# Kernel optimization log

Hardware: AMD Instinct MI355X
Metric: run time of the kernel (lower is better)

The kernel has to match this reference:

```python
import jax, jax.numpy as jnp
import numpy as np

B, T, F, H = 2048, 256, 64, 128


def setup_inputs() -> dict:
    key = jax.random.key(0)
    ks = jax.random.split(key, 9)
    s = 0.1  # small init scale for stable recurrence
    return {
        "x": jax.random.normal(ks[0], (B, T, F), dtype=jnp.float32),
        "W_ih": jax.random.normal(ks[1], (4 * H, F), dtype=jnp.float32) * s,
        "W_hh": jax.random.normal(ks[2], (4 * H, H), dtype=jnp.float32) * s,
        "b_ih": jax.random.normal(ks[3], (4 * H,), dtype=jnp.float32) * s,
        "b_hh": jax.random.normal(ks[4], (4 * H,), dtype=jnp.float32) * s,
        "W1": jax.random.normal(ks[5], (32, H), dtype=jnp.float32) * s,
        "b1": jax.random.normal(ks[6], (32,), dtype=jnp.float32) * s,
        "W2": jax.random.normal(ks[7], (1, 32), dtype=jnp.float32) * s,
        "b2": jax.random.normal(ks[8], (1,), dtype=jnp.float32) * s,
    }


def reference(x, W_ih, W_hh, b_ih, b_hh, W1, b1, W2, b2):
    # Single-layer LSTM (PyTorch gate order i, f, g, o), take last hidden state.
    Bsz, Tlen, _ = x.shape
    Hdim = W_hh.shape[1]
    xt = jnp.swapaxes(x, 0, 1)  # [T, B, F]
    bias = b_ih + b_hh  # [4H]

    def step(carry, xb):
        h, c = carry
        gates = xb @ W_ih.T + h @ W_hh.T + bias  # [B, 4H]
        i, f, g, o = jnp.split(gates, 4, axis=-1)
        i = jax.nn.sigmoid(i)
        f = jax.nn.sigmoid(f)
        g = jnp.tanh(g)
        o = jax.nn.sigmoid(o)
        c = f * c + i * g
        h = o * jnp.tanh(c)
        return (h, c), None

    h0 = jnp.zeros((Bsz, Hdim), dtype=x.dtype)
    c0 = jnp.zeros((Bsz, Hdim), dtype=x.dtype)
    (h_last, _), _ = jax.lax.scan(step, (h0, c0), xt)

    # head: Linear(H,32) -> ReLU -> Linear(32,1) -> Sigmoid -> squeeze(-1)
    z = jax.nn.relu(h_last @ W1.T + b1)
    return jax.nn.sigmoid(z @ W2.T + b2)[:, 0]
```

## Files before the change

### kernel.cpp

```cpp
#include <hip/hip_runtime.h>


#define Bsz   2048
#define Tlen  256
#define Fdim  64
#define Hdim  128
#define ROWS  8
#define NTH   512
#define TILE_E 512
#define NKT   6
#define BUF_E (NKT * TILE_E)

using bf16x8 = __attribute__((ext_vector_type(8))) __bf16;
using f32x4  = __attribute__((ext_vector_type(4))) float;

__device__ __forceinline__ float fast_rcp(float x) {
#if __has_builtin(__builtin_amdgcn_rcpf)
    return __builtin_amdgcn_rcpf(x);
#else
    return 1.0f / x;
#endif
}
__device__ __forceinline__ float fast_exp2(float x) {
#if __has_builtin(__builtin_amdgcn_exp2f)
    return __builtin_amdgcn_exp2f(x);
#else
    return exp2f(x);
#endif
}
#define LOG2E  1.4426950408889634f
#define LOG2E2 2.8853900817779268f

__device__ __forceinline__ bf16x8 cvt8(float4 a, float4 b) {
    bf16x8 r;
    r[0]=(__bf16)a.x; r[1]=(__bf16)a.y; r[2]=(__bf16)a.z; r[3]=(__bf16)a.w;
    r[4]=(__bf16)b.x; r[5]=(__bf16)b.y; r[6]=(__bf16)b.z; r[7]=(__bf16)b.w;
    return r;
}

__device__ __forceinline__ int frag_elem(int row, int k) {
    return (k >> 5) * TILE_E + ((((k >> 3) & 3) * 16 + row) * 8) + (k & 7);
}

__global__ __launch_bounds__(NTH, 2)
void lstm_fused(const float* __restrict__ x,
                const float* __restrict__ W_ih,
                const float* __restrict__ W_hh,
                const float* __restrict__ b_ih,
                const float* __restrict__ b_hh,
                const float* __restrict__ W1,
                const float* __restrict__ b1,
                const float* __restrict__ W2,
                const float* __restrict__ b2,
                float* __restrict__ out)
{
    __shared__ __bf16 Abuf[2][BUF_E];
    __shared__ float  hlast[ROWS * Hdim];
    __shared__ float  zbuf[ROWS * 32];

    const int tid  = threadIdx.x;
    const int w    = tid >> 6;
    const int lane = tid & 63;
    const int quad = lane >> 4;
    const int l16  = lane & 15;
    const int b0   = blockIdx.x * ROWS;
    const bool hiq = (quad >= 2);

    bf16x8 bwx[2][4], bwh[4][4];
    #pragma unroll
    for (int kt = 0; kt < NKT; ++kt) {
        const int k0 = kt * 32 + quad * 8;
        #pragma unroll
        for (int g = 0; g < 4; ++g) {
            const int n = g * Hdim + w * 16 + l16;
            const float* p = (kt < 2) ? (W_ih + (size_t)n * Fdim + k0)
                                      : (W_hh + (size_t)n * Hdim + (k0 - Fdim));
            float4 lo = *(const float4*)p;
            float4 hi = *(const float4*)(p + 4);
            bf16x8 r = cvt8(lo, hi);
            if (kt < 2) bwx[kt][g] = r; else bwh[kt - 2][g] = r;
        }
    }
    f32x4 biasf[4];
    #pragma unroll
    for (int g = 0; g < 4; ++g) {
        const int n = g * Hdim + w * 16 + l16;
        const float bv = b_ih[n] + b_hh[n];
        biasf[g] = (f32x4){bv, bv, bv, bv};
    }

    const bool sx_on  = tid < 256;
    const int  sx_row = tid & 7;
    const int  sx_fp  = (tid >> 3) & 31;
    const int  f0     = 2 * sx_fp;
    const float* xrp  = x + (size_t)(b0 + sx_row) * (Tlen * Fdim) + f0;
    const int sx_e0 = frag_elem(sx_row,     f0);
    const int sx_e1 = frag_elem(sx_row + 8, f0);

    const int r0  = (quad >> 1) * 2;
    const int brb = (quad & 1) * 4 + r0;
    const int hc  = 16 * w + l16;
    const int h_e0a = frag_elem(brb,         Fdim + hc);
    const int h_e0b = frag_elem(brb + 8,     Fdim + hc);
    const int h_e1a = frag_elem(brb + 1,     Fdim + hc);
    const int h_e1b = frag_elem(brb + 1 + 8, Fdim + hc);

    #pragma unroll
    for (int i = 0; i < BUF_E / NTH; ++i)
        Abuf[0][tid + i * NTH] = (__bf16)0.0f;
    __syncthreads();
    float2 xpA = make_float2(0.f, 0.f);
    float2 xpB = make_float2(0.f, 0.f);
    if (sx_on) {
        float2 v1 = *(const float2*)(xrp + Fdim);
        __bf16 a1[2] = {(__bf16)v1.x, (__bf16)v1.y};
        *(uint*)&Abuf[0][sx_e0] = *(uint*)a1;
        *(uint*)&Abuf[0][sx_e1] = *(uint*)a1;
        xpA = *(const float2*)(xrp + 2 * Fdim);
        xpB = *(const float2*)(xrp + 3 * Fdim);
    }
    f32x4 xacc[4];
    {
        const float* x0p = x + (size_t)(b0 + (l16 & 7)) * (Tlen * Fdim) + quad * 8;
        float4 a0 = *(const float4*)(x0p);
        float4 a1 = *(const float4*)(x0p + 4);
        float4 a2 = *(const float4*)(x0p + 32);
        float4 a3 = *(const float4*)(x0p + 36);
        bf16x8 xi0 = cvt8(a0, a1), xi1 = cvt8(a2, a3);
        #pragma unroll
        for (int g = 0; g < 4; ++g) {
            f32x4 tmp = __builtin_amdgcn_mfma_f32_16x16x32_bf16(xi0, bwx[0][g], biasf[g], 0, 0, 0);
            xacc[g]   = __builtin_amdgcn_mfma_f32_16x16x32_bf16(xi1, bwx[1][g], tmp, 0, 0, 0);
        }
    }
    __syncthreads();

    float cc0 = 0.0f, cc1 = 0.0f;

    auto step = [&](int t, const __bf16* __restrict__ rb,
                    __bf16* __restrict__ wbf, float2& xstage) {
        bf16x8 hf[4];
        #pragma unroll
        for (int kt = 0; kt < 4; ++kt)
            hf[kt] = *(const bf16x8*)&rb[(2 + kt) * TILE_E + lane * 8];
        bf16x8 xf0 = *(const bf16x8*)&rb[lane * 8];
        bf16x8 xf1 = *(const bf16x8*)&rb[TILE_E + lane * 8];

        float2 xcur = xstage;
        if (sx_on && (t + 4) < Tlen)
            xstage = *(const float2*)(xrp + (size_t)(t + 4) * Fdim);

        f32x4 acc[4];
        #pragma unroll
        for (int g = 0; g < 4; ++g)
            acc[g] = __builtin_amdgcn_mfma_f32_16x16x32_bf16(hf[0], bwh[0][g], xacc[g], 0, 0, 0);
        #pragma unroll
        for (int kt = 1; kt < 4; ++kt) {
            #pragma unroll
            for (int g = 0; g < 4; ++g)
                acc[g] = __builtin_amdgcn_mfma_f32_16x16x32_bf16(hf[kt], bwh[kt][g], acc[g], 0, 0, 0);
        }

        if ((t + 1) < Tlen) {
            #pragma unroll
            for (int g = 0; g < 4; ++g) {
                f32x4 tmp = __builtin_amdgcn_mfma_f32_16x16x32_bf16(xf0, bwx[0][g], biasf[g], 0, 0, 0);
                xacc[g]   = __builtin_amdgcn_mfma_f32_16x16x32_bf16(xf1, bwx[1][g], tmp, 0, 0, 0);
            }
        }

        if (sx_on && (t + 2) < Tlen) {
            __bf16 xa[2] = {(__bf16)xcur.x, (__bf16)xcur.y};
            *(uint*)&wbf[sx_e0] = *(uint*)xa;
            *(uint*)&wbf[sx_e1] = *(uint*)xa;
        }

        __builtin_amdgcn_sched_barrier(0);

        {
            float gi = hiq ? acc[0][2] : acc[0][0];
            float gf = hiq ? acc[1][2] : acc[1][0];
            float gg = hiq ? acc[2][2] : acc[2][0];
            float go = hiq ? acc[3][2] : acc[3][0];
            float ei = fast_exp2(-LOG2E  * gi);
            float ef = fast_exp2(-LOG2E  * gf);
            float eg = fast_exp2(-LOG2E2 * gg);
            float eo = fast_exp2(-LOG2E  * go);
            float a = 1.0f + ef, b = 1.0f + ei, d = 1.0f + eg;
            float bd  = b * d;
            float num = cc0 * bd + a * (1.0f - eg);
            cc0 = num * fast_rcp(a * bd);
            float ec = fast_exp2(-LOG2E2 * cc0);
            float h  = (1.0f - ec) * fast_rcp((1.0f + eo) * (1.0f + ec));
            __bf16 hb = (__bf16)h;
            wbf[h_e0a] = hb;
            wbf[h_e0b] = hb;
            if (t == Tlen - 1) hlast[brb * Hdim + hc] = h;
        }
        {
            float gi = hiq ? acc[0][3] : acc[0][1];
            float gf = hiq ? acc[1][3] : acc[1][1];
            float gg = hiq ? acc[2][3] : acc[2][1];
            float go = hiq ? acc[3][3] : acc[3][1];
            float ei = fast_exp2(-LOG2E  * gi);
            float ef = fast_exp2(-LOG2E  * gf);
            float eg = fast_exp2(-LOG2E2 * gg);
            float eo = fast_exp2(-LOG2E  * go);
            float a = 1.0f + ef, b = 1.0f + ei, d = 1.0f + eg;
            float bd  = b * d;
            float num = cc1 * bd + a * (1.0f - eg);
            cc1 = num * fast_rcp(a * bd);
            float ec = fast_exp2(-LOG2E2 * cc1);
            float h  = (1.0f - ec) * fast_rcp((1.0f + eo) * (1.0f + ec));
            __bf16 hb = (__bf16)h;
            wbf[h_e1a] = hb;
            wbf[h_e1b] = hb;
            if (t == Tlen - 1) hlast[(brb + 1) * Hdim + hc] = h;
        }

        asm volatile("s_waitcnt lgkmcnt(0)" ::: "memory");
        __builtin_amdgcn_s_barrier();
        __builtin_amdgcn_sched_barrier(0);
    };

    for (int t = 0; t < Tlen; t += 2) {
        step(t,     Abuf[0], Abuf[1], xpA);
        step(t + 1, Abuf[1], Abuf[0], xpB);
    }

    if (tid < ROWS * 32) {
        const int b = tid >> 5, n = tid & 31;
        const float4* w4 = (const float4*)(W1 + n * Hdim);
        const float4* h4 = (const float4*)(hlast + b * Hdim);
        float s = b1[n];
        #pragma unroll
        for (int kk = 0; kk < Hdim / 4; ++kk) {
            float4 wv = w4[kk];
            float4 hv = h4[kk];
            s += wv.x * hv.x + wv.y * hv.y + wv.z * hv.z + wv.w * hv.w;
        }
        zbuf[b * 32 + n] = fmaxf(s, 0.0f);
    }
    __syncthreads();
    if (tid < ROWS) {
        float s = b2[0];
        #pragma unroll
        for (int n = 0; n < 32; ++n) s += zbuf[tid * 32 + n] * W2[n];
        float e = fast_exp2(-LOG2E * s);
        out[b0 + tid] = fast_rcp(1.0f + e);
    }
}

extern "C" void kernel_launch(void* const* d_in, const int* in_sizes, int n_in,
                              void* d_out, int out_size, void* d_ws, size_t ws_size,
                              hipStream_t stream) {
    const float* x    = (const float*)d_in[0];
    const float* W_ih = (const float*)d_in[1];
    const float* W_hh = (const float*)d_in[2];
    const float* b_ih = (const float*)d_in[3];
    const float* b_hh = (const float*)d_in[4];
    const float* W1   = (const float*)d_in[5];
    const float* b1   = (const float*)d_in[6];
    const float* W2   = (const float*)d_in[7];
    const float* b2   = (const float*)d_in[8];
    float* out = (float*)d_out;

    dim3 grid(Bsz / ROWS), block(NTH);
    lstm_fused<<<grid, block, 0, stream>>>(x, W_ih, W_hh, b_ih, b_hh, W1, b1, W2, b2, out);
}
```

Baseline: 342.9 us.

## Load x fragments directly from global into registers instead of staging through LDS

```diff
diff --git a/kernel.cpp b/kernel.cpp
--- a/kernel.cpp
+++ b/kernel.cpp
@@ -8,8 +8,8 @@
 #define ROWS  8
 #define NTH   512
 #define TILE_E 512
-#define NKT   6
-#define BUF_E (NKT * TILE_E)
+#define NKT_H 4
+#define BUF_E (NKT_H * TILE_E)
 
 using bf16x8 = __attribute__((ext_vector_type(8))) __bf16;
 using f32x4  = __attribute__((ext_vector_type(4))) float;
@@ -68,7 +68,7 @@
 
     bf16x8 bwx[2][4], bwh[4][4];
     #pragma unroll
-    for (int kt = 0; kt < NKT; ++kt) {
+    for (int kt = 0; kt < 6; ++kt) {
         const int k0 = kt * 32 + quad * 8;
         #pragma unroll
         for (int g = 0; g < 4; ++g) {
@@ -89,43 +89,35 @@
         biasf[g] = (f32x4){bv, bv, bv, bv};
     }
 
-    const bool sx_on  = tid < 256;
-    const int  sx_row = tid & 7;
-    const int  sx_fp  = (tid >> 3) & 31;
-    const int  f0     = 2 * sx_fp;
-    const float* xrp  = x + (size_t)(b0 + sx_row) * (Tlen * Fdim) + f0;
-    const int sx_e0 = frag_elem(sx_row,     f0);
-    const int sx_e1 = frag_elem(sx_row + 8, f0);
+    const float* xq = x + (size_t)(b0 + (l16 & 7)) * (Tlen * Fdim) + quad * 8;
 
     const int r0  = (quad >> 1) * 2;
     const int brb = (quad & 1) * 4 + r0;
     const int hc  = 16 * w + l16;
-    const int h_e0a = frag_elem(brb,         Fdim + hc);
-    const int h_e0b = frag_elem(brb + 8,     Fdim + hc);
-    const int h_e1a = frag_elem(brb + 1,     Fdim + hc);
-    const int h_e1b = frag_elem(brb + 1 + 8, Fdim + hc);
+    const int h_e0a = frag_elem(brb,         hc);
+    const int h_e0b = frag_elem(brb + 8,     hc);
+    const int h_e1a = frag_elem(brb + 1,     hc);
+    const int h_e1b = frag_elem(brb + 1 + 8, hc);
 
     #pragma unroll
     for (int i = 0; i < BUF_E / NTH; ++i)
         Abuf[0][tid + i * NTH] = (__bf16)0.0f;
-    __syncthreads();
-    float2 xpA = make_float2(0.f, 0.f);
-    float2 xpB = make_float2(0.f, 0.f);
-    if (sx_on) {
-        float2 v1 = *(const float2*)(xrp + Fdim);
-        __bf16 a1[2] = {(__bf16)v1.x, (__bf16)v1.y};
-        *(uint*)&Abuf[0][sx_e0] = *(uint*)a1;
-        *(uint*)&Abuf[0][sx_e1] = *(uint*)a1;
-        xpA = *(const float2*)(xrp + 2 * Fdim);
-        xpB = *(const float2*)(xrp + 3 * Fdim);
+
+    float4 xA0, xA1, xA2, xA3, xB0, xB1, xB2, xB3;
+    xB0 = xB1 = xB2 = xB3 = make_float4(0.f, 0.f, 0.f, 0.f);
+    {
+        const float* p = xq + (size_t)1 * Fdim;
+        xA0 = *(const float4*)(p);
+        xA1 = *(const float4*)(p + 4);
+        xA2 = *(const float4*)(p + 32);
+        xA3 = *(const float4*)(p + 36);
     }
     f32x4 xacc[4];
     {
-        const float* x0p = x + (size_t)(b0 + (l16 & 7)) * (Tlen * Fdim) + quad * 8;
-        float4 a0 = *(const float4*)(x0p);
-        float4 a1 = *(const float4*)(x0p + 4);
-        float4 a2 = *(const float4*)(x0p + 32);
-        float4 a3 = *(const float4*)(x0p + 36);
+        float4 a0 = *(const float4*)(xq);
+        float4 a1 = *(const float4*)(xq + 4);
+        float4 a2 = *(const float4*)(xq + 32);
+        float4 a3 = *(const float4*)(xq + 36);
         bf16x8 xi0 = cvt8(a0, a1), xi1 = cvt8(a2, a3);
         #pragma unroll
         for (int g = 0; g < 4; ++g) {
@@ -138,41 +130,40 @@
     float cc0 = 0.0f, cc1 = 0.0f;
 
     auto step = [&](int t, const __bf16* __restrict__ rb,
-                    __bf16* __restrict__ wbf, float2& xstage) {
+                    __bf16* __restrict__ wbf,
+                    float4& xh0, float4& xh1, float4& xh2, float4& xh3,
+                    float4& xl0, float4& xl1, float4& xl2, float4& xl3) {
         bf16x8 hf[4];
         #pragma unroll
-        for (int kt = 0; kt < 4; ++kt)
-            hf[kt] = *(const bf16x8*)&rb[(2 + kt) * TILE_E + lane * 8];
-        bf16x8 xf0 = *(const bf16x8*)&rb[lane * 8];
-        bf16x8 xf1 = *(const bf16x8*)&rb[TILE_E + lane * 8];
-
-        float2 xcur = xstage;
-        if (sx_on && (t + 4) < Tlen)
-            xstage = *(const float2*)(xrp + (size_t)(t + 4) * Fdim);
+        for (int kt = 0; kt < NKT_H; ++kt)
+            hf[kt] = *(const bf16x8*)&rb[kt * TILE_E + lane * 8];
+
+        if ((t + 2) < Tlen) {
+            const float* p = xq + (size_t)(t + 2) * Fdim;
+            xl0 = *(const float4*)(p);
+            xl1 = *(const float4*)(p + 4);
+            xl2 = *(const float4*)(p + 32);
+            xl3 = *(const float4*)(p + 36);
+        }
 
         f32x4 acc[4];
         #pragma unroll
         for (int g = 0; g < 4; ++g)
             acc[g] = __builtin_amdgcn_mfma_f32_16x16x32_bf16(hf[0], bwh[0][g], xacc[g], 0, 0, 0);
         #pragma unroll
-        for (int kt = 1; kt < 4; ++kt) {
+        for (int kt = 1; kt < NKT_H; ++kt) {
             #pragma unroll
             for (int g = 0; g < 4; ++g)
                 acc[g] = __builtin_amdgcn_mfma_f32_16x16x32_bf16(hf[kt], bwh[kt][g], acc[g], 0, 0, 0);
         }
 
         if ((t + 1) < Tlen) {
+            bf16x8 xi0 = cvt8(xh0, xh1), xi1 = cvt8(xh2, xh3);
             #pragma unroll
             for (int g = 0; g < 4; ++g) {
-                f32x4 tmp = __builtin_amdgcn_mfma_f32_16x16x32_bf16(xf0, bwx[0][g], biasf[g], 0, 0, 0);
-                xacc[g]   = __builtin_amdgcn_mfma_f32_16x16x32_bf16(xf1, bwx[1][g], tmp, 0, 0, 0);
+                f32x4 tmp = __builtin_amdgcn_mfma_f32_16x16x32_bf16(xi0, bwx[0][g], biasf[g], 0, 0, 0);
+                xacc[g]   = __builtin_amdgcn_mfma_f32_16x16x32_bf16(xi1, bwx[1][g], tmp, 0, 0, 0);
             }
-        }
-
-        if (sx_on && (t + 2) < Tlen) {
-            __bf16 xa[2] = {(__bf16)xcur.x, (__bf16)xcur.y};
-            *(uint*)&wbf[sx_e0] = *(uint*)xa;
-            *(uint*)&wbf[sx_e1] = *(uint*)xa;
         }
 
         __builtin_amdgcn_sched_barrier(0);
@@ -224,8 +215,8 @@
     };
 
     for (int t = 0; t < Tlen; t += 2) {
-        step(t,     Abuf[0], Abuf[1], xpA);
-        step(t + 1, Abuf[1], Abuf[0], xpB);
+        step(t,     Abuf[0], Abuf[1], xA0, xA1, xA2, xA3, xB0, xB1, xB2, xB3);
+        step(t + 1, Abuf[1], Abuf[0], xB0, xB1, xB2, xB3, xA0, xA1, xA2, xA3);
     }
 
     if (tid < ROWS * 32) {
```

Result: slower. 503.5 us (+46.9%).

## Batch input projection for two timesteps per MFMA and prescale gate weights

Applied to the files above, without the earlier changes.

```diff
diff --git a/kernel.cpp b/kernel.cpp
--- a/kernel.cpp
+++ b/kernel.cpp
@@ -35,6 +35,12 @@
     bf16x8 r;
     r[0]=(__bf16)a.x; r[1]=(__bf16)a.y; r[2]=(__bf16)a.z; r[3]=(__bf16)a.w;
     r[4]=(__bf16)b.x; r[5]=(__bf16)b.y; r[6]=(__bf16)b.z; r[7]=(__bf16)b.w;
+    return r;
+}
+__device__ __forceinline__ bf16x8 cvt8s(float4 a, float4 b, float s) {
+    bf16x8 r;
+    r[0]=(__bf16)(s*a.x); r[1]=(__bf16)(s*a.y); r[2]=(__bf16)(s*a.z); r[3]=(__bf16)(s*a.w);
+    r[4]=(__bf16)(s*b.x); r[5]=(__bf16)(s*b.y); r[6]=(__bf16)(s*b.z); r[7]=(__bf16)(s*b.w);
     return r;
 }
 
@@ -65,6 +71,7 @@
     const int l16  = lane & 15;
     const int b0   = blockIdx.x * ROWS;
     const bool hiq = (quad >= 2);
+    const int bpaddr = (lane ^ 32) << 2;
 
     bf16x8 bwx[2][4], bwh[4][4];
     #pragma unroll
@@ -72,30 +79,31 @@
         const int k0 = kt * 32 + quad * 8;
         #pragma unroll
         for (int g = 0; g < 4; ++g) {
+            const float s = (g == 2) ? -LOG2E2 : -LOG2E;
             const int n = g * Hdim + w * 16 + l16;
             const float* p = (kt < 2) ? (W_ih + (size_t)n * Fdim + k0)
                                       : (W_hh + (size_t)n * Hdim + (k0 - Fdim));
             float4 lo = *(const float4*)p;
             float4 hi = *(const float4*)(p + 4);
-            bf16x8 r = cvt8(lo, hi);
+            bf16x8 r = cvt8s(lo, hi, s);
             if (kt < 2) bwx[kt][g] = r; else bwh[kt - 2][g] = r;
         }
     }
     f32x4 biasf[4];
     #pragma unroll
     for (int g = 0; g < 4; ++g) {
+        const float s = (g == 2) ? -LOG2E2 : -LOG2E;
         const int n = g * Hdim + w * 16 + l16;
-        const float bv = b_ih[n] + b_hh[n];
+        const float bv = s * (b_ih[n] + b_hh[n]);
         biasf[g] = (f32x4){bv, bv, bv, bv};
     }
 
-    const bool sx_on  = tid < 256;
-    const int  sx_row = tid & 7;
-    const int  sx_fp  = (tid >> 3) & 31;
-    const int  f0     = 2 * sx_fp;
-    const float* xrp  = x + (size_t)(b0 + sx_row) * (Tlen * Fdim) + f0;
-    const int sx_e0 = frag_elem(sx_row,     f0);
-    const int sx_e1 = frag_elem(sx_row + 8, f0);
+    const int  sx_row  = tid & 7;
+    const int  sx_fp   = (tid >> 3) & 31;
+    const int  sx_half = (tid >> 8) & 1;
+    const int  f0      = 2 * sx_fp;
+    const float* xrp   = x + (size_t)(b0 + sx_row) * (Tlen * Fdim) + f0;
+    const int  sx_e    = frag_elem(sx_row + 8 * sx_half, f0);
 
     const int r0  = (quad >> 1) * 2;
     const int brb = (quad & 1) * 4 + r0;
@@ -108,84 +116,40 @@
     #pragma unroll
     for (int i = 0; i < BUF_E / NTH; ++i)
         Abuf[0][tid + i * NTH] = (__bf16)0.0f;
-    __syncthreads();
-    float2 xpA = make_float2(0.f, 0.f);
-    float2 xpB = make_float2(0.f, 0.f);
-    if (sx_on) {
-        float2 v1 = *(const float2*)(xrp + Fdim);
-        __bf16 a1[2] = {(__bf16)v1.x, (__bf16)v1.y};
-        *(uint*)&Abuf[0][sx_e0] = *(uint*)a1;
-        *(uint*)&Abuf[0][sx_e1] = *(uint*)a1;
-        xpA = *(const float2*)(xrp + 2 * Fdim);
-        xpB = *(const float2*)(xrp + 3 * Fdim);
-    }
-    f32x4 xacc[4];
+    float2 xpv = *(const float2*)(xrp + (size_t)(2 + sx_half) * Fdim);
+
+    f32x4 xE[4], xO[4];
     {
-        const float* x0p = x + (size_t)(b0 + (l16 & 7)) * (Tlen * Fdim) + quad * 8;
-        float4 a0 = *(const float4*)(x0p);
-        float4 a1 = *(const float4*)(x0p + 4);
-        float4 a2 = *(const float4*)(x0p + 32);
-        float4 a3 = *(const float4*)(x0p + 36);
+        const float* xg = x + (size_t)(b0 + (l16 & 7)) * (Tlen * Fdim)
+                            + (size_t)(l16 >> 3) * Fdim + quad * 8;
+        float4 a0 = *(const float4*)(xg);
+        float4 a1 = *(const float4*)(xg + 4);
+        float4 a2 = *(const float4*)(xg + 32);
+        float4 a3 = *(const float4*)(xg + 36);
         bf16x8 xi0 = cvt8(a0, a1), xi1 = cvt8(a2, a3);
         #pragma unroll
         for (int g = 0; g < 4; ++g) {
             f32x4 tmp = __builtin_amdgcn_mfma_f32_16x16x32_bf16(xi0, bwx[0][g], biasf[g], 0, 0, 0);
-            xacc[g]   = __builtin_amdgcn_mfma_f32_16x16x32_bf16(xi1, bwx[1][g], tmp, 0, 0, 0);
+            f32x4 P   = __builtin_amdgcn_mfma_f32_16x16x32_bf16(xi1, bwx[1][g], tmp, 0, 0, 0);
+            #pragma unroll
+            for (int e = 0; e < 4; ++e) {
+                float sv = __int_as_float(
+                    __builtin_amdgcn_ds_bpermute(bpaddr, __float_as_int(P[e])));
+                xE[g][e] = hiq ? sv   : P[e];
+                xO[g][e] = hiq ? P[e] : sv;
+            }
         }
     }
     __syncthreads();
 
     float cc0 = 0.0f, cc1 = 0.0f;
 
-    auto step = [&](int t, const __bf16* __restrict__ rb,
-                    __bf16* __restrict__ wbf, float2& xstage) {
-        bf16x8 hf[4];
-        #pragma unroll
-        for (int kt = 0; kt < 4; ++kt)
-            hf[kt] = *(const bf16x8*)&rb[(2 + kt) * TILE_E + lane * 8];
-        bf16x8 xf0 = *(const bf16x8*)&rb[lane * 8];
-        bf16x8 xf1 = *(const bf16x8*)&rb[TILE_E + lane * 8];
-
-        float2 xcur = xstage;
-        if (sx_on && (t + 4) < Tlen)
-            xstage = *(const float2*)(xrp + (size_t)(t + 4) * Fdim);
-
-        f32x4 acc[4];
-        #pragma unroll
-        for (int g = 0; g < 4; ++g)
-            acc[g] = __builtin_amdgcn_mfma_f32_16x16x32_bf16(hf[0], bwh[0][g], xacc[g], 0, 0, 0);
-        #pragma unroll
-        for (int kt = 1; kt < 4; ++kt) {
-            #pragma unroll
-            for (int g = 0; g < 4; ++g)
-                acc[g] = __builtin_amdgcn_mfma_f32_16x16x32_bf16(hf[kt], bwh[kt][g], acc[g], 0, 0, 0);
-        }
-
-        if ((t + 1) < Tlen) {
-            #pragma unroll
-            for (int g = 0; g < 4; ++g) {
-                f32x4 tmp = __builtin_amdgcn_mfma_f32_16x16x32_bf16(xf0, bwx[0][g], biasf[g], 0, 0, 0);
-                xacc[g]   = __builtin_amdgcn_mfma_f32_16x16x32_bf16(xf1, bwx[1][g], tmp, 0, 0, 0);
-            }
-        }
-
-        if (sx_on && (t + 2) < Tlen) {
-            __bf16 xa[2] = {(__bf16)xcur.x, (__bf16)xcur.y};
-            *(uint*)&wbf[sx_e0] = *(uint*)xa;
-            *(uint*)&wbf[sx_e1] = *(uint*)xa;
-        }
-
-        __builtin_amdgcn_sched_barrier(0);
-
+    auto cellmath = [&](int t, f32x4* acc, __bf16* __restrict__ wbf) {
         {
-            float gi = hiq ? acc[0][2] : acc[0][0];
-            float gf = hiq ? acc[1][2] : acc[1][0];
-            float gg = hiq ? acc[2][2] : acc[2][0];
-            float go = hiq ? acc[3][2] : acc[3][0];
-            float ei = fast_exp2(-LOG2E  * gi);
-            float ef = fast_exp2(-LOG2E  * gf);
-            float eg = fast_exp2(-LOG2E2 * gg);
-            float eo = fast_exp2(-LOG2E  * go);
+            float ei = fast_exp2(hiq ? acc[0][2] : acc[0][0]);
+            float ef = fast_exp2(hiq ? acc[1][2] : acc[1][0]);
+            float eg = fast_exp2(hiq ? acc[2][2] : acc[2][0]);
+            float eo = fast_exp2(hiq ? acc[3][2] : acc[3][0]);
             float a = 1.0f + ef, b = 1.0f + ei, d = 1.0f + eg;
             float bd  = b * d;
             float num = cc0 * bd + a * (1.0f - eg);
@@ -198,14 +162,10 @@
             if (t == Tlen - 1) hlast[brb * Hdim + hc] = h;
         }
         {
-            float gi = hiq ? acc[0][3] : acc[0][1];
-            float gf = hiq ? acc[1][3] : acc[1][1];
-            float gg = hiq ? acc[2][3] : acc[2][1];
-            float go = hiq ? acc[3][3] : acc[3][1];
-            float ei = fast_exp2(-LOG2E  * gi);
-            float ef = fast_exp2(-LOG2E  * gf);
-            float eg = fast_exp2(-LOG2E2 * gg);
-            float eo = fast_exp2(-LOG2E  * go);
+            float ei = fast_exp2(hiq ? acc[0][3] : acc[0][1]);
+            float ef = fast_exp2(hiq ? acc[1][3] : acc[1][1]);
+            float eg = fast_exp2(hiq ? acc[2][3] : acc[2][1]);
+            float eo = fast_exp2(hiq ? acc[3][3] : acc[3][1]);
             float a = 1.0f + ef, b = 1.0f + ei, d = 1.0f + eg;
             float bd  = b * d;
             float num = cc1 * bd + a * (1.0f - eg);
@@ -217,15 +177,87 @@
             wbf[h_e1b] = hb;
             if (t == Tlen - 1) hlast[(brb + 1) * Hdim + hc] = h;
         }
+    };
+
+    auto stepE = [&](int t, const __bf16* __restrict__ rb,
+                     __bf16* __restrict__ wbf) {
+        bf16x8 hf[4];
+        #pragma unroll
+        for (int kt = 0; kt < 4; ++kt)
+            hf[kt] = *(const bf16x8*)&rb[(2 + kt) * TILE_E + lane * 8];
+
+        if ((t + 2) < Tlen) {
+            __bf16 xa[2] = {(__bf16)xpv.x, (__bf16)xpv.y};
+            *(uint*)&wbf[sx_e] = *(uint*)xa;
+        }
+        if ((t + 4) < Tlen)
+            xpv = *(const float2*)(xrp + (size_t)(t + 4 + sx_half) * Fdim);
+
+        f32x4 acc[4];
+        #pragma unroll
+        for (int g = 0; g < 4; ++g)
+            acc[g] = __builtin_amdgcn_mfma_f32_16x16x32_bf16(hf[0], bwh[0][g], xE[g], 0, 0, 0);
+        #pragma unroll
+        for (int kt = 1; kt < 4; ++kt) {
+            #pragma unroll
+            for (int g = 0; g < 4; ++g)
+                acc[g] = __builtin_amdgcn_mfma_f32_16x16x32_bf16(hf[kt], bwh[kt][g], acc[g], 0, 0, 0);
+        }
+
+        __builtin_amdgcn_sched_barrier(0);
+        cellmath(t, acc, wbf);
 
         asm volatile("s_waitcnt lgkmcnt(0)" ::: "memory");
         __builtin_amdgcn_s_barrier();
         __builtin_amdgcn_sched_barrier(0);
     };
 
+    auto stepO = [&](int t, const __bf16* __restrict__ rb,
+                     __bf16* __restrict__ wbf) {
+        bf16x8 hf[4];
+        #pragma unroll
+        for (int kt = 0; kt < 4; ++kt)
+            hf[kt] = *(const bf16x8*)&rb[(2 + kt) * TILE_E + lane * 8];
+        bf16x8 xf0 = *(const bf16x8*)&rb[lane * 8];
+        bf16x8 xf1 = *(const bf16x8*)&rb[TILE_E + lane * 8];
+
+        f32x4 acc[4];
+        #pragma unroll
+        for (int g = 0; g < 4; ++g)
+            acc[g] = __builtin_amdgcn_mfma_f32_16x16x32_bf16(hf[0], bwh[0][g], xO[g], 0, 0, 0);
+        #pragma unroll
+        for (int kt = 1; kt < 4; ++kt) {
+            #pragma unroll
+            for (int g = 0; g < 4; ++g)
+                acc[g] = __builtin_amdgcn_mfma_f32_16x16x32_bf16(hf[kt], bwh[kt][g], acc[g], 0, 0, 0);
+        }
+
+        if ((t + 1) < Tlen) {
+            #pragma unroll
+            for (int g = 0; g < 4; ++g) {
+                f32x4 tmp = __builtin_amdgcn_mfma_f32_16x16x32_bf16(xf0, bwx[0][g], biasf[g], 0, 0, 0);
+                f32x4 P   = __builtin_amdgcn_mfma_f32_16x16x32_bf16(xf1, bwx[1][g], tmp, 0, 0, 0);
+                #pragma unroll
+                for (int e = 0; e < 4; ++e) {
+                    float sv = __int_as_float(
+                        __builtin_amdgcn_ds_bpermute(bpaddr, __float_as_int(P[e])));
+                    xE[g][e] = hiq ? sv   : P[e];
+                    xO[g][e] = hiq ? P[e] : sv;
+                }
+            }
+        }
+
+        __builtin_amdgcn_sched_barrier(0);
+        cellmath(t, acc, wbf);
+
+        asm volatile("s_waitcnt lgkmcnt(0)" ::: "memory");
+        __builtin_amdgcn_s_barrier();
+        __builtin_amdgcn_sched_barrier(0);
+    };
+
     for (int t = 0; t < Tlen; t += 2) {
-        step(t,     Abuf[0], Abuf[1], xpA);
-        step(t + 1, Abuf[1], Abuf[0], xpB);
+        stepE(t,     Abuf[0], Abuf[1]);
+        stepO(t + 1, Abuf[1], Abuf[0]);
     }
 
     if (tid < ROWS * 32) {
```

Result: slower. 366.3 us (+6.8%).

## Swap MFMA operand roles, halve threads per block, prescale weights for exp2

Applied to the files above, without the earlier changes.

```diff
diff --git a/kernel.cpp b/kernel.cpp
--- a/kernel.cpp
+++ b/kernel.cpp
@@ -6,12 +6,13 @@
 #define Fdim  64
 #define Hdim  128
 #define ROWS  8
-#define NTH   512
+#define NTH   256
 #define TILE_E 512
 #define NKT   6
 #define BUF_E (NKT * TILE_E)
 
 using bf16x8 = __attribute__((ext_vector_type(8))) __bf16;
+using bf16x4 = __attribute__((ext_vector_type(4))) __bf16;
 using f32x4  = __attribute__((ext_vector_type(4))) float;
 
 __device__ __forceinline__ float fast_rcp(float x) {
@@ -31,18 +32,14 @@
 #define LOG2E  1.4426950408889634f
 #define LOG2E2 2.8853900817779268f
 
-__device__ __forceinline__ bf16x8 cvt8(float4 a, float4 b) {
+__device__ __forceinline__ bf16x8 cvt8s(float4 a, float4 b, float s) {
     bf16x8 r;
-    r[0]=(__bf16)a.x; r[1]=(__bf16)a.y; r[2]=(__bf16)a.z; r[3]=(__bf16)a.w;
-    r[4]=(__bf16)b.x; r[5]=(__bf16)b.y; r[6]=(__bf16)b.z; r[7]=(__bf16)b.w;
+    r[0]=(__bf16)(s*a.x); r[1]=(__bf16)(s*a.y); r[2]=(__bf16)(s*a.z); r[3]=(__bf16)(s*a.w);
+    r[4]=(__bf16)(s*b.x); r[5]=(__bf16)(s*b.y); r[6]=(__bf16)(s*b.z); r[7]=(__bf16)(s*b.w);
     return r;
 }
 
-__device__ __forceinline__ int frag_elem(int row, int k) {
-    return (k >> 5) * TILE_E + ((((k >> 3) & 3) * 16 + row) * 8) + (k & 7);
-}
-
-__global__ __launch_bounds__(NTH, 2)
+__global__ __launch_bounds__(NTH, 1)
 void lstm_fused(const float* __restrict__ x,
                 const float* __restrict__ W_ih,
                 const float* __restrict__ W_hh,
@@ -61,84 +58,87 @@
     const int tid  = threadIdx.x;
     const int w    = tid >> 6;
     const int lane = tid & 63;
-    const int quad = lane >> 4;
+    const int q    = lane >> 4;
     const int l16  = lane & 15;
     const int b0   = blockIdx.x * ROWS;
-    const bool hiq = (quad >= 2);
-
-    bf16x8 bwx[2][4], bwh[4][4];
+
+    bf16x8 bwh[2][4][4];
+    bf16x8 bwx[2][4][2];
+    f32x4  biasf[2][4];
     #pragma unroll
-    for (int kt = 0; kt < NKT; ++kt) {
-        const int k0 = kt * 32 + quad * 8;
-        #pragma unroll
-        for (int g = 0; g < 4; ++g) {
-            const int n = g * Hdim + w * 16 + l16;
-            const float* p = (kt < 2) ? (W_ih + (size_t)n * Fdim + k0)
-                                      : (W_hh + (size_t)n * Hdim + (k0 - Fdim));
-            float4 lo = *(const float4*)p;
-            float4 hi = *(const float4*)(p + 4);
-            bf16x8 r = cvt8(lo, hi);
-            if (kt < 2) bwx[kt][g] = r; else bwh[kt - 2][g] = r;
-        }
-    }
-    f32x4 biasf[4];
+    for (int hb = 0; hb < 2; ++hb) {
+        #pragma unroll
+        for (int j = 0; j < 4; ++j) {
+            const float s  = (j == 2) ? -LOG2E2 : -LOG2E;
+            const int   gb = j * Hdim + (2 * w + hb) * 16;
+            const float* ph = W_hh + (size_t)(gb + l16) * Hdim;
+            #pragma unroll
+            for (int kt = 0; kt < 4; ++kt) {
+                float4 lo = *(const float4*)(ph + kt * 32 + q * 8);
+                float4 hi = *(const float4*)(ph + kt * 32 + q * 8 + 4);
+                bwh[hb][j][kt] = cvt8s(lo, hi, s);
+            }
+            const float* px = W_ih + (size_t)(gb + l16) * Fdim;
+            #pragma unroll
+            for (int kt = 0; kt < 2; ++kt) {
+                float4 lo = *(const float4*)(px + kt * 32 + q * 8);
+                float4 hi = *(const float4*)(px + kt * 32 + q * 8 + 4);
+                bwx[hb][j][kt] = cvt8s(lo, hi, s);
+            }
+            const int be = gb + 4 * q;
+            float4 bi = *(const float4*)(b_ih + be);
+            float4 bh = *(const float4*)(b_hh + be);
+            biasf[hb][j] = (f32x4){s*(bi.x+bh.x), s*(bi.y+bh.y),
+                                   s*(bi.z+bh.z), s*(bi.w+bh.w)};
+        }
+    }
+
+    const int  sb  = tid & 7;
+    const int  f0  = 2 * ((tid >> 3) & 31);
+    const float* xrp = x + (size_t)(b0 + sb) * (Tlen * Fdim) + f0;
+    const int  sx_e = (f0 >> 5) * TILE_E + (((f0 >> 3) & 3) * 16 + sb) * 8 + (f0 & 7);
+
+    const int kh0_0 = (2 * w + 0) * 16 + 4 * q;
+    const int kh0_1 = (2 * w + 1) * 16 + 4 * q;
+    const int wr_e0 = (2 + (kh0_0 >> 5)) * TILE_E + (((kh0_0 >> 3) & 3) * 16 + l16) * 8 + (kh0_0 & 7);
+    const int wr_e1 = (2 + (kh0_1 >> 5)) * TILE_E + (((kh0_1 >> 3) & 3) * 16 + l16) * 8 + (kh0_1 & 7);
+
     #pragma unroll
-    for (int g = 0; g < 4; ++g) {
-        const int n = g * Hdim + w * 16 + l16;
-        const float bv = b_ih[n] + b_hh[n];
-        biasf[g] = (f32x4){bv, bv, bv, bv};
-    }
-
-    const bool sx_on  = tid < 256;
-    const int  sx_row = tid & 7;
-    const int  sx_fp  = (tid >> 3) & 31;
-    const int  f0     = 2 * sx_fp;
-    const float* xrp  = x + (size_t)(b0 + sx_row) * (Tlen * Fdim) + f0;
-    const int sx_e0 = frag_elem(sx_row,     f0);
-    const int sx_e1 = frag_elem(sx_row + 8, f0);
-
-    const int r0  = (quad >> 1) * 2;
-    const int brb = (quad & 1) * 4 + r0;
-    const int hc  = 16 * w + l16;
-    const int h_e0a = frag_elem(brb,         Fdim + hc);
-    const int h_e0b = frag_elem(brb + 8,     Fdim + hc);
-    const int h_e1a = frag_elem(brb + 1,     Fdim + hc);
-    const int h_e1b = frag_elem(brb + 1 + 8, Fdim + hc);
-
+    for (int i = 0; i < 2 * BUF_E / NTH; ++i)
+        ((__bf16*)Abuf)[tid + i * NTH] = (__bf16)0.0f;
+    __syncthreads();
+    {
+        float2 v0 = *(const float2*)(xrp);
+        float2 v1 = *(const float2*)(xrp + Fdim);
+        __bf16 a0[2] = {(__bf16)v0.x, (__bf16)v0.y};
+        __bf16 a1[2] = {(__bf16)v1.x, (__bf16)v1.y};
+        *(uint*)&Abuf[1][sx_e] = *(uint*)a0;
+        *(uint*)&Abuf[0][sx_e] = *(uint*)a1;
+    }
+    float2 xpv = *(const float2*)(xrp + 2 * Fdim);
+    __syncthreads();
+    f32x4 xacc[2][4];
+    {
+        bf16x8 xf0 = *(const bf16x8*)&Abuf[1][lane * 8];
+        bf16x8 xf1 = *(const bf16x8*)&Abuf[1][TILE_E + lane * 8];
+        #pragma unroll
+        for (int hb = 0; hb < 2; ++hb)
+            #pragma unroll
+            for (int j = 0; j < 4; ++j) {
+                f32x4 tmp = __builtin_amdgcn_mfma_f32_16x16x32_bf16(bwx[hb][j][0], xf0, biasf[hb][j], 0, 0, 0);
+                xacc[hb][j] = __builtin_amdgcn_mfma_f32_16x16x32_bf16(bwx[hb][j][1], xf1, tmp, 0, 0, 0);
+            }
+    }
+    __syncthreads();
+
+    float cc[2][4];
     #pragma unroll
-    for (int i = 0; i < BUF_E / NTH; ++i)
-        Abuf[0][tid + i * NTH] = (__bf16)0.0f;
-    __syncthreads();
-    float2 xpA = make_float2(0.f, 0.f);
-    float2 xpB = make_float2(0.f, 0.f);
-    if (sx_on) {
-        float2 v1 = *(const float2*)(xrp + Fdim);
-        __bf16 a1[2] = {(__bf16)v1.x, (__bf16)v1.y};
-        *(uint*)&Abuf[0][sx_e0] = *(uint*)a1;
-        *(uint*)&Abuf[0][sx_e1] = *(uint*)a1;
-        xpA = *(const float2*)(xrp + 2 * Fdim);
-        xpB = *(const float2*)(xrp + 3 * Fdim);
-    }
-    f32x4 xacc[4];
-    {
-        const float* x0p = x + (size_t)(b0 + (l16 & 7)) * (Tlen * Fdim) + quad * 8;
-        float4 a0 = *(const float4*)(x0p);
-        float4 a1 = *(const float4*)(x0p + 4);
-        float4 a2 = *(const float4*)(x0p + 32);
-        float4 a3 = *(const float4*)(x0p + 36);
-        bf16x8 xi0 = cvt8(a0, a1), xi1 = cvt8(a2, a3);
-        #pragma unroll
-        for (int g = 0; g < 4; ++g) {
-            f32x4 tmp = __builtin_amdgcn_mfma_f32_16x16x32_bf16(xi0, bwx[0][g], biasf[g], 0, 0, 0);
-            xacc[g]   = __builtin_amdgcn_mfma_f32_16x16x32_bf16(xi1, bwx[1][g], tmp, 0, 0, 0);
-        }
-    }
-    __syncthreads();
-
-    float cc0 = 0.0f, cc1 = 0.0f;
+    for (int hb = 0; hb < 2; ++hb)
+        #pragma unroll
+        for (int e = 0; e < 4; ++e) cc[hb][e] = 0.0f;
 
     auto step = [&](int t, const __bf16* __restrict__ rb,
-                    __bf16* __restrict__ wbf, float2& xstage) {
+                    __bf16* __restrict__ wbf) {
         bf16x8 hf[4];
         #pragma unroll
         for (int kt = 0; kt < 4; ++kt)
@@ -146,76 +146,66 @@
         bf16x8 xf0 = *(const bf16x8*)&rb[lane * 8];
         bf16x8 xf1 = *(const bf16x8*)&rb[TILE_E + lane * 8];
 
-        float2 xcur = xstage;
-        if (sx_on && (t + 4) < Tlen)
-            xstage = *(const float2*)(xrp + (size_t)(t + 4) * Fdim);
-
-        f32x4 acc[4];
-        #pragma unroll
-        for (int g = 0; g < 4; ++g)
-            acc[g] = __builtin_amdgcn_mfma_f32_16x16x32_bf16(hf[0], bwh[0][g], xacc[g], 0, 0, 0);
-        #pragma unroll
-        for (int kt = 1; kt < 4; ++kt) {
-            #pragma unroll
-            for (int g = 0; g < 4; ++g)
-                acc[g] = __builtin_amdgcn_mfma_f32_16x16x32_bf16(hf[kt], bwh[kt][g], acc[g], 0, 0, 0);
-        }
+        float2 xcur = xpv;
+        if ((t + 3) < Tlen)
+            xpv = *(const float2*)(xrp + (size_t)(t + 3) * Fdim);
+
+        f32x4 acc[2][4];
+        #pragma unroll
+        for (int hb = 0; hb < 2; ++hb)
+            #pragma unroll
+            for (int j = 0; j < 4; ++j)
+                acc[hb][j] = __builtin_amdgcn_mfma_f32_16x16x32_bf16(bwh[hb][j][0], hf[0], xacc[hb][j], 0, 0, 0);
+        #pragma unroll
+        for (int kt = 1; kt < 4; ++kt)
+            #pragma unroll
+            for (int hb = 0; hb < 2; ++hb)
+                #pragma unroll
+                for (int j = 0; j < 4; ++j)
+                    acc[hb][j] = __builtin_amdgcn_mfma_f32_16x16x32_bf16(bwh[hb][j][kt], hf[kt], acc[hb][j], 0, 0, 0);
 
         if ((t + 1) < Tlen) {
             #pragma unroll
-            for (int g = 0; g < 4; ++g) {
-                f32x4 tmp = __builtin_amdgcn_mfma_f32_16x16x32_bf16(xf0, bwx[0][g], biasf[g], 0, 0, 0);
-                xacc[g]   = __builtin_amdgcn_mfma_f32_16x16x32_bf16(xf1, bwx[1][g], tmp, 0, 0, 0);
-            }
-        }
-
-        if (sx_on && (t + 2) < Tlen) {
+            for (int hb = 0; hb < 2; ++hb)
+                #pragma unroll
+                for (int j = 0; j < 4; ++j) {
+                    f32x4 tmp = __builtin_amdgcn_mfma_f32_16x16x32_bf16(bwx[hb][j][0], xf0, biasf[hb][j], 0, 0, 0);
+                    xacc[hb][j] = __builtin_amdgcn_mfma_f32_16x16x32_bf16(bwx[hb][j][1], xf1, tmp, 0, 0, 0);
+                }
+        }
+
+        if ((t + 2) < Tlen) {
             __bf16 xa[2] = {(__bf16)xcur.x, (__bf16)xcur.y};
-            *(uint*)&wbf[sx_e0] = *(uint*)xa;
-            *(uint*)&wbf[sx_e1] = *(uint*)xa;
+            *(uint*)&wbf[sx_e] = *(uint*)xa;
         }
 
         __builtin_amdgcn_sched_barrier(0);
 
-        {
-            float gi = hiq ? acc[0][2] : acc[0][0];
-            float gf = hiq ? acc[1][2] : acc[1][0];
-            float gg = hiq ? acc[2][2] : acc[2][0];
-            float go = hiq ? acc[3][2] : acc[3][0];
-            float ei = fast_exp2(-LOG2E  * gi);
-            float ef = fast_exp2(-LOG2E  * gf);
-            float eg = fast_exp2(-LOG2E2 * gg);
-            float eo = fast_exp2(-LOG2E  * go);
-            float a = 1.0f + ef, b = 1.0f + ei, d = 1.0f + eg;
-            float bd  = b * d;
-            float num = cc0 * bd + a * (1.0f - eg);
-            cc0 = num * fast_rcp(a * bd);
-            float ec = fast_exp2(-LOG2E2 * cc0);
-            float h  = (1.0f - ec) * fast_rcp((1.0f + eo) * (1.0f + ec));
-            __bf16 hb = (__bf16)h;
-            wbf[h_e0a] = hb;
-            wbf[h_e0b] = hb;
-            if (t == Tlen - 1) hlast[brb * Hdim + hc] = h;
-        }
-        {
-            float gi = hiq ? acc[0][3] : acc[0][1];
-            float gf = hiq ? acc[1][3] : acc[1][1];
-            float gg = hiq ? acc[2][3] : acc[2][1];
-            float go = hiq ? acc[3][3] : acc[3][1];
-            float ei = fast_exp2(-LOG2E  * gi);
-            float ef = fast_exp2(-LOG2E  * gf);
-            float eg = fast_exp2(-LOG2E2 * gg);
-            float eo = fast_exp2(-LOG2E  * go);
-            float a = 1.0f + ef, b = 1.0f + ei, d = 1.0f + eg;
-            float bd  = b * d;
-            float num = cc1 * bd + a * (1.0f - eg);
-            cc1 = num * fast_rcp(a * bd);
-            float ec = fast_exp2(-LOG2E2 * cc1);
-            float h  = (1.0f - ec) * fast_rcp((1.0f + eo) * (1.0f + ec));
-            __bf16 hb = (__bf16)h;
-            wbf[h_e1a] = hb;
-            wbf[h_e1b] = hb;
-            if (t == Tlen - 1) hlast[(brb + 1) * Hdim + hc] = h;
+        #pragma unroll
+        for (int hb = 0; hb < 2; ++hb) {
+            bf16x4 hv;
+            float  hl[4];
+            #pragma unroll
+            for (int e = 0; e < 4; ++e) {
+                float ei = fast_exp2(acc[hb][0][e]);
+                float ef = fast_exp2(acc[hb][1][e]);
+                float eg = fast_exp2(acc[hb][2][e]);
+                float eo = fast_exp2(acc[hb][3][e]);
+                float a = 1.0f + ef, b = 1.0f + ei, d = 1.0f + eg;
+                float bd  = b * d;
+                float num = cc[hb][e] * bd + a * (1.0f - eg);
+                float c   = num * fast_rcp(a * bd);
+                cc[hb][e] = c;
+                float ec = fast_exp2(-LOG2E2 * c);
+                float h  = (1.0f - ec) * fast_rcp((1.0f + eo) * (1.0f + ec));
+                hv[e] = (__bf16)h;
+                hl[e] = h;
+            }
+            *(bf16x4*)&wbf[hb ? wr_e1 : wr_e0] = hv;
+            if (t == Tlen - 1 && l16 < 8) {
+                *(float4*)&hlast[l16 * Hdim + (hb ? kh0_1 : kh0_0)] =
+                    make_float4(hl[0], hl[1], hl[2], hl[3]);
+            }
         }
 
         asm volatile("s_waitcnt lgkmcnt(0)" ::: "memory");
@@ -224,11 +214,11 @@
     };
 
     for (int t = 0; t < Tlen; t += 2) {
-        step(t,     Abuf[0], Abuf[1], xpA);
-        step(t + 1, Abuf[1], Abuf[0], xpB);
-    }
-
-    if (tid < ROWS * 32) {
+        step(t,     Abuf[0], Abuf[1]);
+        step(t + 1, Abuf[1], Abuf[0]);
+    }
+
+    {
         const int b = tid >> 5, n = tid & 31;
         const float4* w4 = (const float4*)(W1 + n * Hdim);
         const float4* h4 = (const float4*)(hlast + b * Hdim);
```

After: 417.6 us. +21.8%, slower.
